# Kernel tuning notes

Measured on AMD Instinct MI355X. Metric: run time of the kernel, lower is better.

## Reference

```python
import jax, jax.numpy as jnp
import numpy as np
from functools import partial

B_, L_, H_, DIN_, K_, N_, R_ = 2, 2048, 1024, 2048, 4, 16, 64

def setup_inputs() -> dict:
    key = jax.random.key(0)
    ks = jax.random.split(key, 9)
    s = lambda f: 1.0 / f ** 0.5
    A = jnp.tile(jnp.arange(1, N_ + 1, dtype=jnp.float32)[None, :], (DIN_, 1))
    return {
        'hidden_states': jax.random.normal(ks[0], (B_, L_, H_), jnp.float32),
        'w_in':   jax.random.normal(ks[1], (2 * DIN_, H_), jnp.float32) * s(H_),
        'w_conv': jax.random.normal(ks[2], (DIN_, 1, K_), jnp.float32) * s(DIN_),
        'w_xproj': jax.random.normal(ks[3], (R_ + 2 * N_, DIN_), jnp.float32) * s(DIN_),
        'w_dt':   jax.random.normal(ks[4], (DIN_, R_), jnp.float32) * s(R_),
        'b_dt':   jnp.zeros((DIN_,), jnp.float32),
        'A_log':  jnp.log(A),
        'D':      jnp.ones((DIN_,), jnp.float32),
        'w_out':  jax.random.normal(ks[5], (H_, DIN_), jnp.float32) * s(DIN_),
    }

def _selective_scan(x, delta, A, Bm, Cm, D):
    # x, delta: [b,l,d]; A: [d,n]; Bm, Cm: [b,l,n]; D: [d]
    dA  = jnp.exp(jnp.einsum('bld,dn->bldn', delta, A))      # [b,l,d,n]
    dBx = jnp.einsum('bld,bln->bldn', delta * x, Bm)          # [b,l,d,n]
    b, l, d, n = dA.shape
    def step(z, inp):
        dA_t, dBx_t, c_t = inp                                # [b,d,n],[b,d,n],[b,n]
        z = dA_t * z + dBx_t
        y = jnp.einsum('bdn,bn->bd', z, c_t)
        return z, y
    z0 = jnp.zeros((b, d, n), x.dtype)
    _, ys = jax.lax.scan(step, z0, (jnp.moveaxis(dA, 1, 0), jnp.moveaxis(dBx, 1, 0), jnp.moveaxis(Cm, 1, 0)))
    y = jnp.moveaxis(ys, 0, 1)                                # [b,l,d]
    return y + x * D

def reference(hidden_states, w_in, w_conv, w_xproj, w_dt, b_dt, A_log, D, w_out):
    b, l, h = hidden_states.shape
    d_in, n = A_log.shape
    hs_res = hidden_states @ w_in.T                           # [b,l,2*d_in]
    hs, res = hs_res[..., :d_in], hs_res[..., d_in:]
    # depthwise causal conv1d: pad k-1 left (padding=k-1 then [:l] slice)
    xc = jnp.moveaxis(hs, 1, 2)                               # [b,d_in,l]
    xc = jax.lax.conv_general_dilated(xc, w_conv, window_strides=(1,),
                                      padding=[(K_ - 1, 0)],
                                      dimension_numbers=('NCH', 'OIH', 'NCH'),
                                      feature_group_count=d_in)
    hs = jax.nn.silu(jnp.moveaxis(xc, 1, 2))                  # [b,l,d_in]
    A = -jnp.exp(A_log)
    x_dbl = hs @ w_xproj.T                                    # [b,l,r+2n]
    dt, Bm, Cm = x_dbl[..., :R_], x_dbl[..., R_:R_ + n], x_dbl[..., R_ + n:]
    delta = jax.nn.softplus(dt @ w_dt.T + b_dt)               # [b,l,d_in]
    y = _selective_scan(hs, delta, A, Bm, Cm, D)
    y = y * jax.nn.silu(res)
    return y @ w_out.T
```

## Files before the change

kernel.cpp:

```cpp
#include <hip/hip_runtime.h>
#include <hip/hip_bf16.h>
#include <stdint.h>

#define B_    2
#define L_    2048
#define H_    1024
#define DIN_  2048
#define NST   16
#define RD    64
#define M_    (B_*L_)
#define LC    64
#define NCH   32

typedef __attribute__((ext_vector_type(8))) short short8;
typedef __attribute__((ext_vector_type(4))) float f32x4;

__device__ inline ushort f2bf(float v) {
  uint32_t u = __float_as_uint(v);
  uint32_t r = (u + 0x7fffu + ((u >> 16) & 1u)) >> 16;
  return (ushort)r;
}
__device__ inline float bf2f(ushort h) { return __uint_as_float(((uint32_t)h) << 16); }

__device__ inline void gload_lds16(const ushort* g, ushort* l) {
  __builtin_amdgcn_global_load_lds((const __attribute__((address_space(1))) void*)g,
                                   (__attribute__((address_space(3))) void*)l, 16, 0, 0);
}

__global__ __launch_bounds__(256)
void pack_hilo(const float* __restrict__ in, ushort* __restrict__ out,
               int rows, int cols, int in_stride, int out_rows)
{
  int half = cols >> 1;
  int idx = blockIdx.x * 256 + threadIdx.x;
  if (idx >= out_rows * half) return;
  int r = idx / half;
  int c = (idx - r * half) * 2;
  float v0 = 0.f, v1 = 0.f;
  if (r < rows) { const float* p = in + (size_t)r * in_stride + c; v0 = p[0]; v1 = p[1]; }
  ushort h0 = f2bf(v0), h1 = f2bf(v1);
  ushort g0 = f2bf(v0 - bf2f(h0)), g1 = f2bf(v1 - bf2f(h1));
  ushort* orow = out + (size_t)r * (2 * cols);
  *(uint32_t*)(orow + c)        = (uint32_t)h0 | ((uint32_t)h1 << 16);
  *(uint32_t*)(orow + cols + c) = (uint32_t)g0 | ((uint32_t)g1 << 16);
}

template<int EPI>
__global__ __launch_bounds__(256, 4)
void gemm_bt(const ushort* __restrict__ A, const ushort* __restrict__ Bw,
             float* __restrict__ C, int M, int N, int K,
             const float* __restrict__ bias)
{
  const int P = 2 * K;
  const int Kp = 3 * K;
  __shared__ ushort sA[2][128 * 32];
  __shared__ ushort sB[2][128 * 32];
  const int tid = threadIdx.x, wid = tid >> 6, lid = tid & 63;
  const size_t m0 = (size_t)blockIdx.x * 128, n0 = (size_t)blockIdx.y * 128;
  int kLen = Kp, kBase = 0;
  if (gridDim.z > 1) { kLen = Kp / gridDim.z; kBase = blockIdx.z * kLen; C += (size_t)blockIdx.z * M * N; }
  const int nIter = kLen / 32;

  const ushort* gA[2]; const ushort* gB[2];
  ushort* lA[2]; ushort* lB[2];
#pragma unroll
  for (int t = 0; t < 2; ++t) {
    int j = wid * 2 + t;
    gA[t] = A  + (size_t)(m0 + j * 16 + (lid >> 2)) * P + (lid & 3) * 8;
    gB[t] = Bw + (size_t)(n0 + j * 16 + (lid >> 2)) * P + (lid & 3) * 8;
    lA[t] = &sA[0][j * 512];
    lB[t] = &sB[0][j * 512];
  }

  f32x4 acc[4][4];
#pragma unroll
  for (int i = 0; i < 4; ++i)
#pragma unroll
    for (int j = 0; j < 4; ++j) acc[i][j] = (f32x4){0.f, 0.f, 0.f, 0.f};

  {
    int kk = kBase;
    int kA = kk < P ? kk : kk - P;
    int kB = kk < K ? kk : kk - K;
#pragma unroll
    for (int t = 0; t < 2; ++t) { gload_lds16(gA[t] + kA, lA[t]); gload_lds16(gB[t] + kB, lB[t]); }
  }

  const int wr = wid >> 1, wc = wid & 1;
  const int arow = wr * 64 + (lid & 15), brow = wc * 64 + (lid & 15);
  const int fofs = (lid >> 4) * 8;
  int buf = 0;
  for (int it = 0; it < nIter; ++it) {
    __syncthreads();
    if (it + 1 < nIter) {
      int kk = kBase + (it + 1) * 32;
      int kA = kk < P ? kk : kk - P;
      int kB = kk < K ? kk : kk - K;
      int nb = buf ^ 1;
#pragma unroll
      for (int t = 0; t < 2; ++t) {
        gload_lds16(gA[t] + kA, lA[t] + nb * 4096);
        gload_lds16(gB[t] + kB, lB[t] + nb * 4096);
      }
    }
    short8 af[4], bfr[4];
    const ushort* pa = &sA[buf][arow * 32 + fofs];
    const ushort* pb = &sB[buf][brow * 32 + fofs];
#pragma unroll
    for (int i = 0; i < 4; ++i) af[i] = *(const short8*)(pa + i * 16 * 32);
#pragma unroll
    for (int j = 0; j < 4; ++j) bfr[j] = *(const short8*)(pb + j * 16 * 32);
#pragma unroll
    for (int i = 0; i < 4; ++i)
#pragma unroll
      for (int j = 0; j < 4; ++j)
        acc[i][j] = __builtin_amdgcn_mfma_f32_16x16x32_bf16(af[i], bfr[j], acc[i][j], 0, 0, 0);
    buf ^= 1;
  }

  const int crow = (lid >> 4) * 4, ccol = lid & 15;
#pragma unroll
  for (int i = 0; i < 4; ++i) {
    size_t row = m0 + wr * 64 + i * 16 + crow;
#pragma unroll
    for (int j = 0; j < 4; ++j) {
      size_t col = n0 + wc * 64 + j * 16 + ccol;
#pragma unroll
      for (int r = 0; r < 4; ++r) {
        float v = acc[i][j][r];
        if (EPI == 1) { v += bias[col]; v = (v > 20.f) ? v : __logf(1.f + __expf(v)); }
        C[(row + r) * N + col] = v;
      }
    }
  }
}

__global__ __launch_bounds__(256)
void reduce2_out(const float* __restrict__ part, float* __restrict__ out)
{
  int i = blockIdx.x * 256 + threadIdx.x;
  const f32x4* p0 = (const f32x4*)part;
  const f32x4* p1 = (const f32x4*)(part + (size_t)M_ * 1024);
  f32x4 a = p0[i], b = p1[i];
  ((f32x4*)out)[i] = (f32x4){a.x + b.x, a.y + b.y, a.z + b.z, a.w + b.w};
}

#define CONV_LT 8
__global__ __launch_bounds__(256)
void conv_silu_pack(const float* __restrict__ hs_res, const float* __restrict__ w_conv,
                    ushort* __restrict__ hsc_pk)
{
  const int d = blockIdx.x * 256 + threadIdx.x;
  const int l0 = blockIdx.y * CONV_LT;
  const int b = blockIdx.z;
  const float w0 = w_conv[d * 4 + 0], w1 = w_conv[d * 4 + 1];
  const float w2 = w_conv[d * 4 + 2], w3 = w_conv[d * 4 + 3];
  const float* in = hs_res + (size_t)(b * L_) * 4096 + d;
  float a0 = 0.f, a1 = 0.f, a2 = 0.f;
  if (l0 > 0) {
    a0 = in[(size_t)(l0 - 3) * 4096];
    a1 = in[(size_t)(l0 - 2) * 4096];
    a2 = in[(size_t)(l0 - 1) * 4096];
  }
#pragma unroll
  for (int t = 0; t < CONV_LT; ++t) {
    int l = l0 + t;
    float x = in[(size_t)l * 4096];
    float v = fmaf(w0, a0, fmaf(w1, a1, fmaf(w2, a2, w3 * x)));
    v = v / (1.f + __expf(-v));
    size_t m = (size_t)b * L_ + l;
    ushort hi = f2bf(v), lo = f2bf(v - bf2f(hi));
    hsc_pk[m * 4096 + d] = hi;
    hsc_pk[m * 4096 + 2048 + d] = lo;
    a0 = a1; a1 = a2; a2 = x;
  }
}

__global__ __launch_bounds__(256)
void reduce_xdbl(const float* __restrict__ part, float* __restrict__ x_dbl,
                 ushort* __restrict__ dt_pk)
{
  int i = blockIdx.x * 256 + threadIdx.x;
  float s = 0.f;
#pragma unroll
  for (int z = 0; z < 16; ++z) s += part[(size_t)z * (M_ * 128) + i];
  x_dbl[i] = s;
  int c = i & 127, r = i >> 7;
  if (c < 64) {
    ushort hi = f2bf(s), lo = f2bf(s - bf2f(hi));
    dt_pk[(size_t)r * 128 + c] = hi;
    dt_pk[(size_t)r * 128 + 64 + c] = lo;
  }
}

__global__ __launch_bounds__(256)
void scan_pass1(const ushort* __restrict__ hsc_pk, const float* __restrict__ delta,
                const float* __restrict__ x_dbl, const float* __restrict__ A_log,
                float* __restrict__ Pbuf, float* __restrict__ Qbuf)
{
  __shared__ float sBC[LC * 32];
  const int d = blockIdx.x * 256 + threadIdx.x;
  const int c = blockIdx.y, b = blockIdx.z;
  const int l0 = c * LC;
#pragma unroll
  for (int q = 0; q < 8; ++q) {
    int f = threadIdx.x + 256 * q;
    int lr = f >> 5, nn = f & 31;
    sBC[f] = x_dbl[((size_t)(b * L_ + l0 + lr)) * 128 + 64 + nn];
  }
  float An[NST];
#pragma unroll
  for (int n = 0; n < NST; ++n) An[n] = -__expf(A_log[(size_t)d * 16 + n]);
  float z[NST], Pp[NST];
#pragma unroll
  for (int n = 0; n < NST; ++n) { z[n] = 0.f; Pp[n] = 1.f; }
  __syncthreads();
  const float*  dp = delta  + (size_t)(b * L_ + l0) * 2048 + d;
  const ushort* xp = hsc_pk + (size_t)(b * L_ + l0) * 4096 + d;
  for (int t = 0; t < LC; ++t) {
    float dl = dp[(size_t)t * 2048];
    float xv = bf2f(xp[(size_t)t * 4096]) + bf2f(xp[(size_t)t * 4096 + 2048]);
    float dx = dl * xv;
    const float* bc = &sBC[t * 32];
#pragma unroll
    for (int n = 0; n < NST; ++n) {
      float dA = __expf(dl * An[n]);
      z[n] = fmaf(dA, z[n], dx * bc[n]);
      Pp[n] *= dA;
    }
  }
  size_t base = ((size_t)(b * NCH + c) * 16) * 2048 + d;
#pragma unroll
  for (int n = 0; n < NST; ++n) {
    Pbuf[base + (size_t)n * 2048] = Pp[n];
    Qbuf[base + (size_t)n * 2048] = z[n];
  }
}

__global__ __launch_bounds__(256)
void scan_combine(const float* __restrict__ Pbuf, const float* __restrict__ Qbuf,
                  float* __restrict__ zinit)
{
  int i = blockIdx.x * 256 + threadIdx.x;
  int d = i & 2047, n = (i >> 11) & 15, b = i >> 15;
  float z = 0.f;
  for (int c = 0; c < NCH; ++c) {
    size_t idx = ((size_t)(b * NCH + c) * 16 + n) * 2048 + d;
    zinit[idx] = z;
    z = fmaf(Pbuf[idx], z, Qbuf[idx]);
  }
}

__global__ __launch_bounds__(256)
void scan_pass2(ushort* __restrict__ hsc_pk, const float* __restrict__ delta,
                const float* __restrict__ x_dbl, const float* __restrict__ A_log,
                const float* __restrict__ zinit, const float* __restrict__ Dvec,
                const float* __restrict__ hs_res)
{
  __shared__ float sBC[LC * 32];
  const int d = blockIdx.x * 256 + threadIdx.x;
  const int c = blockIdx.y, b = blockIdx.z;
  const int l0 = c * LC;
#pragma unroll
  for (int q = 0; q < 8; ++q) {
    int f = threadIdx.x + 256 * q;
    int lr = f >> 5, nn = f & 31;
    sBC[f] = x_dbl[((size_t)(b * L_ + l0 + lr)) * 128 + 64 + nn];
  }
  float An[NST];
#pragma unroll
  for (int n = 0; n < NST; ++n) An[n] = -__expf(A_log[(size_t)d * 16 + n]);
  float z[NST];
  size_t zb = ((size_t)(b * NCH + c) * 16) * 2048 + d;
#pragma unroll
  for (int n = 0; n < NST; ++n) z[n] = zinit[zb + (size_t)n * 2048];
  const float Dd = Dvec[d];
  __syncthreads();
  const float* dp = delta  + (size_t)(b * L_ + l0) * 2048 + d;
  ushort*      xp = hsc_pk + (size_t)(b * L_ + l0) * 4096 + d;
  const float* rp = hs_res + (size_t)(b * L_ + l0) * 4096 + 2048 + d;
  for (int t = 0; t < LC; ++t) {
    float dl = dp[(size_t)t * 2048];
    float xv = bf2f(xp[(size_t)t * 4096]) + bf2f(xp[(size_t)t * 4096 + 2048]);
    float dx = dl * xv;
    const float* bc = &sBC[t * 32];
    float y = 0.f;
#pragma unroll
    for (int n = 0; n < NST; ++n) {
      float dA = __expf(dl * An[n]);
      z[n] = fmaf(dA, z[n], dx * bc[n]);
      y = fmaf(z[n], bc[16 + n], y);
    }
    y = fmaf(xv, Dd, y);
    float rv = rp[(size_t)t * 4096];
    y *= rv / (1.f + __expf(-rv));
    ushort hi = f2bf(y), lo = f2bf(y - bf2f(hi));
    xp[(size_t)t * 4096] = hi;
    xp[(size_t)t * 4096 + 2048] = lo;
  }
}

extern "C" void kernel_launch(void* const* d_in, const int* in_sizes, int n_in,
                              void* d_out, int out_size, void* d_ws, size_t ws_size,
                              hipStream_t stream)
{
  (void)in_sizes; (void)n_in; (void)out_size; (void)ws_size;
  const float* hidden  = (const float*)d_in[0];
  const float* w_in    = (const float*)d_in[1];
  const float* w_conv  = (const float*)d_in[2];
  const float* w_xproj = (const float*)d_in[3];
  const float* w_dt    = (const float*)d_in[4];
  const float* b_dt    = (const float*)d_in[5];
  const float* A_log   = (const float*)d_in[6];
  const float* Dvec    = (const float*)d_in[7];
  const float* w_out   = (const float*)d_in[8];
  float* out = (float*)d_out;

  char* ws = (char*)d_ws;
  size_t off = 0;
  auto alloc = [&](size_t bytes) -> char* {
    char* p = ws + off; off += (bytes + 255) & ~(size_t)255; return p;
  };
  ushort* w_out_pk = (ushort*)alloc((size_t)1024 * 4096 * 2);
  float*  hs_res   = (float*) alloc((size_t)4096 * 4096 * 4);
  ushort* hsc_pk   = (ushort*)alloc((size_t)4096 * 4096 * 2);
  float*  delta    = (float*) alloc((size_t)4096 * 2048 * 4);
  char*   regA     = alloc((size_t)16 * 1024 * 1024);
  char*   regB     = alloc((size_t)16 * 1024 * 1024);
  ushort* w_xproj_pk = (ushort*)alloc((size_t)128 * 4096 * 2);
  ushort* w_dt_pk    = (ushort*)alloc((size_t)2048 * 128 * 2);
  ushort* dt_pk      = (ushort*)alloc((size_t)4096 * 128 * 2);
  float*  x_dbl      = (float*) alloc((size_t)4096 * 128 * 4);

  ushort* hsin_pk   = (ushort*)regA;
  float*  Pbuf      = (float*)regA;
  float*  Qbuf      = (float*)(regA + 8 * 1024 * 1024);
  ushort* w_in_pk   = (ushort*)regB;
  float*  zinit     = (float*)regB;
  float*  xdbl_part = delta;
  float*  out_part  = hs_res;
  ushort* y_pk      = hsc_pk;

  auto packBlocks = [](int out_rows, int cols) { return (out_rows * (cols / 2) + 255) / 256; };

  pack_hilo<<<packBlocks(4096, 1024), 256, 0, stream>>>(hidden, hsin_pk, 4096, 1024, 1024, 4096);
  pack_hilo<<<packBlocks(4096, 1024), 256, 0, stream>>>(w_in, w_in_pk, 4096, 1024, 1024, 4096);
  pack_hilo<<<packBlocks(128, 2048), 256, 0, stream>>>(w_xproj, w_xproj_pk, 96, 2048, 2048, 128);
  pack_hilo<<<packBlocks(2048, 64), 256, 0, stream>>>(w_dt, w_dt_pk, 2048, 64, 64, 2048);
  pack_hilo<<<packBlocks(1024, 2048), 256, 0, stream>>>(w_out, w_out_pk, 1024, 2048, 2048, 1024);

  gemm_bt<0><<<dim3(32, 32, 1), 256, 0, stream>>>(hsin_pk, w_in_pk, hs_res, 4096, 4096, 1024, nullptr);

  conv_silu_pack<<<dim3(8, L_ / CONV_LT, B_), 256, 0, stream>>>(hs_res, w_conv, hsc_pk);

  gemm_bt<0><<<dim3(32, 1, 16), 256, 0, stream>>>(hsc_pk, w_xproj_pk, xdbl_part, 4096, 128, 2048, nullptr);
  reduce_xdbl<<<(4096 * 128) / 256, 256, 0, stream>>>(xdbl_part, x_dbl, dt_pk);

  gemm_bt<1><<<dim3(32, 16, 1), 256, 0, stream>>>(dt_pk, w_dt_pk, delta, 4096, 2048, 64, b_dt);

  scan_pass1<<<dim3(8, NCH, B_), 256, 0, stream>>>(hsc_pk, delta, x_dbl, A_log, Pbuf, Qbuf);
  scan_combine<<<(B_ * 16 * 2048) / 256, 256, 0, stream>>>(Pbuf, Qbuf, zinit);
  scan_pass2<<<dim3(8, NCH, B_), 256, 0, stream>>>(hsc_pk, delta, x_dbl, A_log, zinit, Dvec, hs_res);

  gemm_bt<0><<<dim3(32, 8, 2), 256, 0, stream>>>(y_pk, w_out_pk, out_part, 4096, 1024, 2048, nullptr);
  reduce2_out<<<(4096 * 1024 / 4) / 256, 256, 0, stream>>>(out_part, out);
}
```

Baseline: 465.6 us.

## Add 256x256-tile 8-wave pipelined GEMM for in_proj and out_proj

Adds a new GEMM kernel with 256x256 output tiles, 512 threads, a double-buffered LDS ring with async global-to-LDS staging interleaved between MFMA phases, and priority hints. It replaces the 128x128 GEMM for the input projection and for the output projection; the output projection now uses a 4-way split-K with a 4-input reduction. The goal is more operand reuse per LDS byte and better overlap of loads with MFMA work. In exchange it raises register and LDS pressure, gives fewer blocks for the in_proj grid (256 blocks), and makes the split-K partial buffer and its reduction larger.

```diff
diff --git a/kernel.cpp b/kernel.cpp
--- a/kernel.cpp
+++ b/kernel.cpp
@@ -45,6 +45,125 @@
   *(uint32_t*)(orow + cols + c) = (uint32_t)g0 | ((uint32_t)g1 << 16);
 }
 
+__device__ __forceinline__ void stage256(const ushort* __restrict__ Gm, size_t rowBase,
+                                         int P, int K, int isB, int kkBase,
+                                         ushort* dstRegion, int tid)
+{
+#pragma unroll
+  for (int r = 0; r < 2; ++r) {
+    int u = r * 512 + tid;
+    int kgrp = u >> 8;
+    int rowL = u & 255;
+    int kk = kkBase + kgrp * 8;
+    int ph = isB ? (kk < K ? kk : kk - K) : (kk < 2 * K ? kk : kk - 2 * K);
+    const ushort* src = Gm + (rowBase + rowL) * (size_t)P + ph;
+    ushort* dst = dstRegion + kgrp * 2048 + (rowL & ~63) * 8;
+    gload_lds16(src, dst);
+  }
+}
+
+#define NOSTG ((void)0)
+#define PH_SYNC(VMSTR) \
+  __builtin_amdgcn_sched_barrier(0); \
+  asm volatile("s_waitcnt vmcnt(" VMSTR ")" ::: "memory"); \
+  __builtin_amdgcn_s_barrier(); \
+  __builtin_amdgcn_sched_barrier(0);
+
+#define PH_EVEN(VMSTR, BUF, KS, STG) { \
+  PH_SYNC(VMSTR) \
+  const ushort* ap_ = lds + (BUF)*32768 + (KS)*8192 + kg*2048 + (wr*128 + lr)*8; \
+  const ushort* bp_ = lds + (BUF)*32768 + 16384 + (KS)*8192 + kg*2048 + (wc*64 + lr)*8; \
+  short8 av[4]; \
+  _Pragma("unroll") for (int f_ = 0; f_ < 4; ++f_) av[f_] = *(const short8*)(ap_ + f_*128); \
+  _Pragma("unroll") for (int g_ = 0; g_ < 4; ++g_) bv[g_] = *(const short8*)(bp_ + g_*128); \
+  STG; \
+  __builtin_amdgcn_s_setprio(1); \
+  _Pragma("unroll") for (int f_ = 0; f_ < 4; ++f_) \
+    _Pragma("unroll") for (int g_ = 0; g_ < 4; ++g_) \
+      acc[f_][g_] = __builtin_amdgcn_mfma_f32_16x16x32_bf16(av[f_], bv[g_], acc[f_][g_], 0, 0, 0); \
+  __builtin_amdgcn_s_setprio(0); }
+
+#define PH_ODD(VMSTR, BUF, KS, STG) { \
+  PH_SYNC(VMSTR) \
+  const ushort* ap_ = lds + (BUF)*32768 + (KS)*8192 + kg*2048 + (wr*128 + 64 + lr)*8; \
+  short8 av[4]; \
+  _Pragma("unroll") for (int f_ = 0; f_ < 4; ++f_) av[f_] = *(const short8*)(ap_ + f_*128); \
+  STG; \
+  __builtin_amdgcn_s_setprio(1); \
+  _Pragma("unroll") for (int f_ = 0; f_ < 4; ++f_) \
+    _Pragma("unroll") for (int g_ = 0; g_ < 4; ++g_) \
+      acc[4+f_][g_] = __builtin_amdgcn_mfma_f32_16x16x32_bf16(av[f_], bv[g_], acc[4+f_][g_], 0, 0, 0); \
+  __builtin_amdgcn_s_setprio(0); }
+
+__global__ __launch_bounds__(512, 2)
+void gemm256(const ushort* __restrict__ A, const ushort* __restrict__ Bw,
+             float* __restrict__ C, int M, int N, int K)
+{
+  __shared__ ushort lds[65536];
+  const int tid = threadIdx.x;
+  const int lid = tid & 63, wid = tid >> 6;
+  const int kg = lid >> 4, lr = lid & 15;
+  const int wr = wid >> 2, wc = wid & 3;
+  const int P = 2 * K, Kp = 3 * K;
+  const size_t m0 = (size_t)blockIdx.x * 256, n0 = (size_t)blockIdx.y * 256;
+  int kLen = Kp, kBase = 0;
+  if (gridDim.z > 1) { kLen /= (int)gridDim.z; kBase = blockIdx.z * kLen; C += (size_t)blockIdx.z * M * N; }
+  const int nt = kLen / 64, J = nt / 2;
+
+  f32x4 acc[8][4];
+#pragma unroll
+  for (int i = 0; i < 8; ++i)
+#pragma unroll
+    for (int j = 0; j < 4; ++j) acc[i][j] = (f32x4){0.f, 0.f, 0.f, 0.f};
+
+  stage256(A,  m0, P, K, 0, kBase +  0, lds + 0,             tid);
+  stage256(Bw, n0, P, K, 1, kBase +  0, lds + 16384,         tid);
+  stage256(A,  m0, P, K, 0, kBase + 32, lds + 8192,          tid);
+  stage256(Bw, n0, P, K, 1, kBase + 32, lds + 16384 + 8192,  tid);
+  stage256(A,  m0, P, K, 0, kBase + 64, lds + 32768,         tid);
+  stage256(Bw, n0, P, K, 1, kBase + 64, lds + 32768 + 16384, tid);
+  asm volatile("s_waitcnt vmcnt(0)" ::: "memory");
+
+  short8 bv[4];
+  for (int j = 0; j < J - 1; ++j) {
+    const int t1k = kBase + (2 * j + 1) * 64;
+    const int t2k = kBase + (2 * j + 2) * 64;
+    const int t3k = kBase + (2 * j + 3) * 64;
+    PH_EVEN("8", 0, 0, stage256(A,  m0, P, K, 0, t1k + 32, lds + 32768 + 8192,         tid));
+    PH_ODD ("8", 0, 0, stage256(Bw, n0, P, K, 1, t1k + 32, lds + 32768 + 16384 + 8192, tid));
+    PH_EVEN("8", 0, 1, stage256(A,  m0, P, K, 0, t2k,      lds + 0,                    tid));
+    PH_ODD ("8", 0, 1, stage256(Bw, n0, P, K, 1, t2k,      lds + 16384,                tid));
+    PH_EVEN("8", 1, 0, stage256(A,  m0, P, K, 0, t2k + 32, lds + 8192,                 tid));
+    PH_ODD ("8", 1, 0, stage256(Bw, n0, P, K, 1, t2k + 32, lds + 16384 + 8192,         tid));
+    PH_EVEN("8", 1, 1, stage256(A,  m0, P, K, 0, t3k,      lds + 32768,                tid));
+    PH_ODD ("8", 1, 1, stage256(Bw, n0, P, K, 1, t3k,      lds + 32768 + 16384,        tid));
+  }
+  {
+    const int t1k = kBase + (nt - 1) * 64;
+    PH_EVEN("8", 0, 0, stage256(A,  m0, P, K, 0, t1k + 32, lds + 32768 + 8192,         tid));
+    PH_ODD ("8", 0, 0, stage256(Bw, n0, P, K, 1, t1k + 32, lds + 32768 + 16384 + 8192, tid));
+    PH_EVEN("8", 0, 1, NOSTG);
+    PH_ODD ("8", 0, 1, NOSTG);
+    PH_EVEN("4", 1, 0, NOSTG);
+    PH_ODD ("4", 1, 0, NOSTG);
+    PH_EVEN("0", 1, 1, NOSTG);
+    PH_ODD ("0", 1, 1, NOSTG);
+  }
+
+  const int crow = (lid >> 4) * 4;
+#pragma unroll
+  for (int mi = 0; mi < 8; ++mi) {
+    size_t row = m0 + wr * 128 + (mi >> 2) * 64 + (mi & 3) * 16 + crow;
+#pragma unroll
+    for (int g = 0; g < 4; ++g) {
+      size_t col = n0 + (size_t)wc * 64 + g * 16 + lr;
+#pragma unroll
+      for (int rr = 0; rr < 4; ++rr)
+        C[(row + rr) * N + col] = acc[mi][g][rr];
+    }
+  }
+}
+
 template<int EPI>
 __global__ __launch_bounds__(256, 4)
 void gemm_bt(const ushort* __restrict__ A, const ushort* __restrict__ Bw,
@@ -136,13 +255,16 @@
 }
 
 __global__ __launch_bounds__(256)
-void reduce2_out(const float* __restrict__ part, float* __restrict__ out)
+void reduce4_out(const float* __restrict__ part, float* __restrict__ out)
 {
   int i = blockIdx.x * 256 + threadIdx.x;
   const f32x4* p0 = (const f32x4*)part;
   const f32x4* p1 = (const f32x4*)(part + (size_t)M_ * 1024);
-  f32x4 a = p0[i], b = p1[i];
-  ((f32x4*)out)[i] = (f32x4){a.x + b.x, a.y + b.y, a.z + b.z, a.w + b.w};
+  const f32x4* p2 = (const f32x4*)(part + (size_t)2 * M_ * 1024);
+  const f32x4* p3 = (const f32x4*)(part + (size_t)3 * M_ * 1024);
+  f32x4 a = p0[i], b = p1[i], c = p2[i], d = p3[i];
+  ((f32x4*)out)[i] = (f32x4){a.x + b.x + c.x + d.x, a.y + b.y + c.y + d.y,
+                             a.z + b.z + c.z + d.z, a.w + b.w + c.w + d.w};
 }
 
 #define CONV_LT 8
@@ -205,8 +327,8 @@
 #pragma unroll
   for (int q = 0; q < 8; ++q) {
     int f = threadIdx.x + 256 * q;
-    int lr = f >> 5, nn = f & 31;
-    sBC[f] = x_dbl[((size_t)(b * L_ + l0 + lr)) * 128 + 64 + nn];
+    int lrr = f >> 5, nn = f & 31;
+    sBC[f] = x_dbl[((size_t)(b * L_ + l0 + lrr)) * 128 + 64 + nn];
   }
   float An[NST];
 #pragma unroll
@@ -264,8 +386,8 @@
 #pragma unroll
   for (int q = 0; q < 8; ++q) {
     int f = threadIdx.x + 256 * q;
-    int lr = f >> 5, nn = f & 31;
-    sBC[f] = x_dbl[((size_t)(b * L_ + l0 + lr)) * 128 + 64 + nn];
+    int lrr = f >> 5, nn = f & 31;
+    sBC[f] = x_dbl[((size_t)(b * L_ + l0 + lrr)) * 128 + 64 + nn];
   }
   float An[NST];
 #pragma unroll
@@ -349,7 +471,7 @@
   pack_hilo<<<packBlocks(2048, 64), 256, 0, stream>>>(w_dt, w_dt_pk, 2048, 64, 64, 2048);
   pack_hilo<<<packBlocks(1024, 2048), 256, 0, stream>>>(w_out, w_out_pk, 1024, 2048, 2048, 1024);
 
-  gemm_bt<0><<<dim3(32, 32, 1), 256, 0, stream>>>(hsin_pk, w_in_pk, hs_res, 4096, 4096, 1024, nullptr);
+  gemm256<<<dim3(16, 16, 1), 512, 0, stream>>>(hsin_pk, w_in_pk, hs_res, 4096, 4096, 1024);
 
   conv_silu_pack<<<dim3(8, L_ / CONV_LT, B_), 256, 0, stream>>>(hs_res, w_conv, hsc_pk);
 
@@ -362,6 +484,6 @@
   scan_combine<<<(B_ * 16 * 2048) / 256, 256, 0, stream>>>(Pbuf, Qbuf, zinit);
   scan_pass2<<<dim3(8, NCH, B_), 256, 0, stream>>>(hsc_pk, delta, x_dbl, A_log, zinit, Dvec, hs_res);
 
-  gemm_bt<0><<<dim3(32, 8, 2), 256, 0, stream>>>(y_pk, w_out_pk, out_part, 4096, 1024, 2048, nullptr);
-  reduce2_out<<<(4096 * 1024 / 4) / 256, 256, 0, stream>>>(out_part, out);
-}
+  gemm256<<<dim3(16, 4, 4), 512, 0, stream>>>(y_pk, w_out_pk, out_part, 4096, 1024, 2048);
+  reduce4_out<<<(4096 * 1024 / 4) / 256, 256, 0, stream>>>(out_part, out);
+}
```

New measurement: 480.9 us. 3.3% more time.
